# Performance work log

Hardware: AMD Instinct MI355X
Metric: run time of the kernel (lower is better)

The kernel has to match this reference:

```python
import jax, jax.numpy as jnp
import numpy as np

PLAYERS = 8
DMODEL = 256          # cfg.dmodel (per-embedding dim)
DK = 1024             # cfg.dk
WINDOW = 4096         # cfg.window == T here
A_SPACE = 64
DFULL = DMODEL * 2 * PLAYERS   # 4096, the concatenated model dim


def _positional_encoding(T, dmodel):
    # i = 1/10000^(2j/dmodel); pe[:, ::2]=sin(pos*i), pe[:, 1::2]=cos(pos*i)
    i = 1.0 / jnp.power(jnp.float32(10000.0), jnp.arange(0, dmodel, 2, dtype=jnp.float32) / dmodel)
    pos = jnp.arange(T, dtype=jnp.float32)[:, None]
    pe = jnp.zeros((T, dmodel), dtype=jnp.float32)
    pe = pe.at[:, ::2].set(jnp.sin(pos * i))
    pe = pe.at[:, 1::2].set(jnp.cos(pos * i))
    return pe


def setup_inputs() -> dict:
    key = jax.random.key(0)
    ks = jax.random.split(key, 12)
    n_rows = WINDOW * 2 * PLAYERS  # 65536 one-hot rows
    idx = jax.random.randint(ks[0], (n_rows,), 0, PLAYERS + 1)
    obs = jax.nn.one_hot(idx, PLAYERS + 1, dtype=jnp.int32)
    std = 2.0 / (5.0 * DFULL)  # torch.normal(0, var) uses var as std in the source
    return {
        "obs": obs,
        "o_emb": jax.random.normal(ks[1], (PLAYERS + 1, DMODEL), jnp.float32),
        "d_emb": jax.random.normal(ks[2], (PLAYERS + 1, DMODEL), jnp.float32),
        "WQ": jax.random.normal(ks[3], (DFULL, DK), jnp.float32) * std,
        "WK": jax.random.normal(ks[4], (DFULL, DK), jnp.float32) * std,
        "WV": jax.random.normal(ks[5], (DFULL, DK), jnp.float32) * std,
        "WO": jax.random.normal(ks[6], (DK, DK), jnp.float32) * std,
        "Wo_pol": jax.random.normal(ks[7], (A_SPACE, DK), jnp.float32) * 0.02,
        "bo_pol": jnp.zeros((A_SPACE,), jnp.float32),
        "Wd_pol": jax.random.normal(ks[8], (A_SPACE, DK), jnp.float32) * 0.02,
        "bd_pol": jnp.zeros((A_SPACE,), jnp.float32),
        "Wv": jax.random.normal(ks[9], (1, DK), jnp.float32) * 0.02,
        "bv": jnp.zeros((1,), jnp.float32),
    }


def reference(obs, o_emb, d_emb, WQ, WK, WV, WO, Wo_pol, bo_pol, Wd_pol, bd_pol, Wv, bv):
    obs2 = obs.reshape(-1, PLAYERS + 1)
    # torch.where(row == 1)[1] on one-hot rows == argmax
    idx_o = jnp.argmax(obs2[::2], axis=1)   # [T*players]
    idx_d = jnp.argmax(obs2[1::2], axis=1)  # [T*players]
    emb = jnp.concatenate([o_emb[idx_o], d_emb[idx_d]], axis=1)  # [T*players, 2*dmodel]
    x = emb.reshape(-1, DFULL) * jnp.sqrt(jnp.float32(DMODEL))    # [T, DFULL]
    T = x.shape[0]
    x = x + _positional_encoding(T, DFULL)
    q = x @ WQ  # [T, DK]
    k = x @ WK
    v = x @ WV
    att = jax.nn.softmax((q @ k.T) / jnp.sqrt(jnp.float32(DK)), axis=-1)  # [T, T]
    o = (att @ v) @ WO  # [T, DK]
    h = jax.nn.relu(o[-1])  # last position only, [DK]
    o_logits = h @ Wo_pol.T + bo_pol  # [A_SPACE]
    d_logits = h @ Wd_pol.T + bd_pol  # [A_SPACE]
    value = h @ Wv.T + bv             # [1]
    return (o_logits, d_logits, value)
```

## Files before the change

### kernel.cpp

```cpp
#include <hip/hip_runtime.h>
#include <stdint.h>

#define DK      1024
#define NBLK    256
#define NT      1024
#define NBAR    5u
#define LOG2_10000 13.287712379549449f

__device__ float g_e[4096];
__device__ float g_kq[4096];
__device__ float g_ol[1024];
__device__ float g_q8[2][8][1024];
__device__ float g_ctx8[2][8][1024];
__device__ float g_w8[2][8][160];

__device__ unsigned bar_gc[256];
__device__ unsigned bar_gm[32];
__device__ unsigned bar_gen;

__device__ __forceinline__ void stg(float* p, float v) {
    __hip_atomic_store(p, v, __ATOMIC_RELAXED, __HIP_MEMORY_SCOPE_AGENT);
}
__device__ __forceinline__ float lda(const float* p) {
    return __hip_atomic_load(p, __ATOMIC_RELAXED, __HIP_MEMORY_SCOPE_AGENT);
}

__device__ __forceinline__ void gbar_arrive(int bid, unsigned target) {
    asm volatile("s_waitcnt vmcnt(0)" ::: "memory");
    __syncthreads();
    if (threadIdx.x == 0) {
        unsigned g = (unsigned)bid & 7u;
        unsigned old = __hip_atomic_fetch_add(&bar_gc[g * 32], 1u,
                           __ATOMIC_RELAXED, __HIP_MEMORY_SCOPE_AGENT);
        if (old == target * 32u - 1u) {
            unsigned o2 = __hip_atomic_fetch_add(&bar_gm[0], 1u,
                              __ATOMIC_RELAXED, __HIP_MEMORY_SCOPE_AGENT);
            if (o2 == target * 8u - 1u)
                __hip_atomic_store(&bar_gen, target, __ATOMIC_RELEASE,
                                   __HIP_MEMORY_SCOPE_AGENT);
        }
    }
}
__device__ __forceinline__ void gbar_wait(unsigned target) {
    if (threadIdx.x == 0) {
        int gd = 0;
        while (__hip_atomic_load(&bar_gen, __ATOMIC_RELAXED,
                                 __HIP_MEMORY_SCOPE_AGENT) < target) {
            __builtin_amdgcn_s_sleep(1);
            if (++gd > (1 << 17)) break;
        }
    }
    __syncthreads();
}
__device__ __forceinline__ void gbar(int bid, unsigned target) {
    gbar_arrive(bid, target);
    gbar_wait(target);
}

__device__ __forceinline__ float4 bred4(float4 a, float* buf, int tid) {
    #pragma unroll
    for (int off = 32; off; off >>= 1) {
        a.x += __shfl_down(a.x, off, 64);
        a.y += __shfl_down(a.y, off, 64);
        a.z += __shfl_down(a.z, off, 64);
        a.w += __shfl_down(a.w, off, 64);
    }
    float4* b4 = (float4*)buf;
    if ((tid & 63) == 0) b4[tid >> 6] = a;
    __syncthreads();
    float4 r = {0.f, 0.f, 0.f, 0.f};
    if (tid == 0) {
        #pragma unroll
        for (int i = 0; i < 16; ++i) {
            float4 t = b4[i];
            r.x += t.x; r.y += t.y; r.z += t.z; r.w += t.w;
        }
    }
    __syncthreads();
    return r;
}

__global__ __launch_bounds__(1024, 4) void fused_k(
        const int*   __restrict__ obs,
        const float* __restrict__ o_emb,  const float* __restrict__ d_emb,
        const float* __restrict__ WQ,     const float* __restrict__ WK,
        const float* __restrict__ WV,     const float* __restrict__ WO,
        const float* __restrict__ Wo_pol, const float* __restrict__ bo_pol,
        const float* __restrict__ Wd_pol, const float* __restrict__ bd_pol,
        const float* __restrict__ Wv,     const float* __restrict__ bv,
        float* __restrict__ out,          char* __restrict__ ws) {
    (void)ws;

    __shared__ __align__(16) float smem[12416];
    float* axpeL = &smem[12288];
    unsigned char* sidx = (unsigned char*)&smem[12304];
    unsigned* sgen = (unsigned*)&smem[12400];

    int bid = blockIdx.x, tid = threadIdx.x;
    const int w  = ((bid & 7) << 5) | (bid >> 3);
    const int sh = bid & 7;
    const int lane = tid & 63;
    const int ksub = tid >> 8, n4 = tid & 255;

    if (tid == 0)
        *sgen = __hip_atomic_load(&bar_gen, __ATOMIC_RELAXED,
                                  __HIP_MEMORY_SCOPE_AGENT);

    const float4* WQ4 = (const float4*)WQ;
    float4 wqr[4];
    #pragma unroll
    for (int kk = 0; kk < 4; ++kk)
        wqr[kk] = WQ4[(size_t)(w * 16 + ksub * 4 + kk) * 256 + n4];

    int*   lidx = (int*)&smem[4100];
    float* lx   = &smem[4120];
    if (tid < 256) {
        int g = w * 256 + tid;
        const int* r = obs + (size_t)g * 9;
        int id = 0;
        #pragma unroll
        for (int j = 1; j < 9; ++j) id += j * r[j];
        sidx[(tid & ~15) | ((tid & 1) << 3) | ((tid >> 1) & 7)] =
            (unsigned char)id;
    }
    if (tid < 16) {
        const int* rr = obs + (size_t)(65520 + tid) * 9;
        int id2 = 0;
        #pragma unroll
        for (int j = 1; j < 9; ++j) id2 += j * rr[j];
        lidx[(tid & 1) * 8 + (tid >> 1)] = id2;
    }
    __syncthreads();
    const unsigned gen0 = *sgen;
    const int par = (int)((gen0 / NBAR) & 1u);
    float* q8  = &g_q8[par][0][0];
    float* c8  = &g_ctx8[par][0][0];
    float* w8  = &g_w8[par][0][0];
    {
        float* q8n = &g_q8[par ^ 1][0][0];
        float* c8n = &g_ctx8[par ^ 1][0][0];
        float* w8n = &g_w8[par ^ 1][0][0];
        if (tid < 69) {
            int idx = w * 69 + tid;
            if (idx < 8192)       stg(&q8n[idx], 0.0f);
            else if (idx < 16384) stg(&c8n[idx - 8192], 0.0f);
            else                  stg(&w8n[idx - 16384], 0.0f);
        }
    }
    if (tid < 16) {
        int c = w * 16 + tid;
        int p = c >> 9, rr = c & 511;
        const float* tab = (rr < 256) ? o_emb : d_emb;
        int slot = (rr < 256) ? p : 8 + p;
        int r2 = rr & 255;
        float e = tab[lidx[slot] * 256 + r2];
        float f = exp2f(-((float)(c & ~1) * (1.0f / 4096.0f)) * LOG2_10000);
        float sv, cv;
        __sincosf(4095.0f * f, &sv, &cv);
        lx[tid] = e * 16.0f + ((c & 1) ? cv : sv);
    }
    __syncthreads();
    {
        float4 acc = {0.f, 0.f, 0.f, 0.f};
        #pragma unroll
        for (int kk = 0; kk < 4; ++kk) {
            float xv = lx[ksub * 4 + kk];
            acc.x += xv * wqr[kk].x; acc.y += xv * wqr[kk].y;
            acc.z += xv * wqr[kk].z; acc.w += xv * wqr[kk].w;
        }
        float4* p4 = (float4*)smem;
        p4[ksub * 256 + n4] = acc;
        __syncthreads();
        if (tid < 256) {
            float4 a = p4[tid], b = p4[256 + tid],
                   c2 = p4[512 + tid], d = p4[768 + tid];
            float* dst = &q8[sh * 1024 + tid * 4];
            atomicAdd(dst + 0, a.x + b.x + c2.x + d.x);
            atomicAdd(dst + 1, a.y + b.y + c2.y + d.y);
            atomicAdd(dst + 2, a.z + b.z + c2.z + d.z);
            atomicAdd(dst + 3, a.w + b.w + c2.w + d.w);
        }
    }
    float4 wkr[4];
    {
        const float4* WKr = (const float4*)(WK + (size_t)(w * 16 + (tid >> 6)) * DK);
        #pragma unroll
        for (int i = 0; i < 4; ++i) wkr[i] = WKr[i * 64 + lane];
    }
    gbar_arrive(bid, gen0 + 1);
    {
        float* lemb = &smem[4096];
        float* lfrq = &smem[8724];
        for (int i = tid; i < 2048; i += NT)
            lfrq[i] = exp2f(-((float)(2 * i) * (1.0f / 4096.0f)) * LOG2_10000);
        for (int i = tid; i < 4608; i += NT) {
            int row = i >> 8, r = i & 255;
            lemb[row * 257 + r] = (row < 9) ? o_emb[row * 256 + r]
                                            : d_emb[(row - 9) * 256 + r];
        }
    }
    gbar_wait(gen0 + 1);

    {
        float* qsum = &smem[10772];
        float t = 0.0f;
        #pragma unroll
        for (int s2 = 0; s2 < 8; ++s2) t += lda(&q8[s2 * 1024 + tid]);
        qsum[tid] = t;
        __syncthreads();
        const float4* q4 = (const float4*)qsum;
        float acc = 0.0f;
        #pragma unroll
        for (int i = 0; i < 4; ++i) {
            float4 qq = q4[i * 64 + lane];
            acc += wkr[i].x * qq.x + wkr[i].y * qq.y
                 + wkr[i].z * qq.z + wkr[i].w * qq.w;
        }
        #pragma unroll
        for (int off = 32; off; off >>= 1) acc += __shfl_down(acc, off, 64);
        if (lane == 0) stg(&g_kq[w * 16 + (tid >> 6)], acc * (1.0f / 32.0f));
    }
    gbar(bid, gen0 + 2);

    {
        float* lkq   = smem;
        float* lemb  = &smem[4096];
        float* lfrq  = &smem[8724];
        float* ldot4 = &smem[10772];
        float* le16  = &smem[11360];
        float* lped  = &smem[11380];
        float* lh    = &smem[11400];
        #pragma unroll
        for (int i = 0; i < 4; ++i) {
            int c = tid + NT * i;
            lkq[c] = lda(&g_kq[c]);
        }
        if (tid < 144) lh[tid] = 0.0f;
        __syncthreads();
        if (tid < 576) {
            int p = tid >> 2, q = tid & 3;
            int sg = p / 9, id = p % 9;
            int base = (sg < 8) ? sg * 512 : (sg - 8) * 512 + 256;
            const float* e = lemb + ((sg < 8) ? id : (9 + id)) * 257;
            float a = 0.0f;
            for (int i = 0; i < 64; ++i) {
                int r = q * 64 + ((i + q * 13) & 63);
                a += e[r] * lkq[base + r];
            }
            ldot4[tid] = a;
        }
        {
            int tt = tid >> 6;
            int t = w * 16 + tt;
            float acc = 0.0f;
            #pragma unroll 4
            for (int jj = 0; jj < 32; ++jj) {
                int jf = jj * 64 + lane;
                float f = lfrq[jf];
                float svv, cvv;
                __sincosf((float)t * f, &svv, &cvv);
                acc += svv * lkq[2 * jf] + cvv * lkq[2 * jf + 1];
            }
            #pragma unroll
            for (int off = 32; off; off >>= 1) acc += __shfl_down(acc, off, 64);
            if (lane == 0) lped[tt] = acc;
        }
        __syncthreads();
        if (tid < 16) {
            float tot = lped[tid];
            const uint32_t* ip = (const uint32_t*)(sidx + tid * 16);
            uint32_t u0 = ip[0], u1 = ip[1], u2 = ip[2], u3 = ip[3];
            #pragma unroll
            for (int sg = 0; sg < 16; ++sg) {
                uint32_t u = (sg < 4) ? u0 : (sg < 8) ? u1 : (sg < 12) ? u2 : u3;
                int id = (u >> ((sg & 3) * 8)) & 0xFF;
                int p = (sg * 9 + id) * 4;
                tot += 16.0f * (ldot4[p] + ldot4[p + 1] + ldot4[p + 2] + ldot4[p + 3]);
            }
            float e = expf(tot);
            le16[tid] = e;
            stg(&g_e[w * 16 + tid], e);
        }
        __syncthreads();
        if (tid < 256) {
            int lt = tid >> 4, seg = tid & 15;
            int id = sidx[lt * 16 + seg];
            atomicAdd(&lh[seg * 9 + id], le16[lt]);
        }
        __syncthreads();
        if (tid < 144) atomicAdd(&w8[sh * 160 + tid], lh[tid]);
    }
    gbar(bid, gen0 + 3);

    float4 wvr[4];
    {
        const float4* WV4 = (const float4*)WV;
        #pragma unroll
        for (int kk = 0; kk < 4; ++kk)
            wvr[kk] = WV4[(size_t)(w * 16 + ksub * 4 + kk) * 256 + n4];
    }
    {
        float* le  = smem;
        float* pss = &smem[4352];
        float* psc = &smem[5376];
        float* lw  = &smem[6400];
        float* axv = &smem[6576];
        #pragma unroll
        for (int i = 0; i < 4; ++i) {
            int c = tid + NT * i;
            le[c] = lda(&g_e[c]);
        }
        if (tid < 144) {
            float s = 0.0f;
            #pragma unroll
            for (int s2 = 0; s2 < 8; ++s2) s += lda(&w8[s2 * 160 + tid]);
            lw[tid] = s;
        }
        __syncthreads();
        {
            int jl = tid >> 7, ts = tid & 127;
            int j = w * 8 + jl;
            float f = exp2f(-((float)(2 * j) * (1.0f / 4096.0f)) * LOG2_10000);
            float sf, cf;
            __sincosf(f, &sf, &cf);
            int t0 = ts * 32;
            float sv, cv;
            __sincosf((float)t0 * f, &sv, &cv);
            float ss = 0.f, sc = 0.f;
            #pragma unroll
            for (int i = 0; i < 32; ++i) {
                float a = le[t0 + i];
                ss += a * sv; sc += a * cv;
                float ns = sv * cf + cv * sf;
                cv = cv * cf - sv * sf;
                sv = ns;
            }
            pss[tid] = ss; psc[tid] = sc;
        }
        __syncthreads();
        if (tid < 512) {
            int m2 = tid >> 6, l = tid & 63;
            float a  = pss[m2 * 128 + l] + pss[m2 * 128 + 64 + l];
            float b2 = psc[m2 * 128 + l] + psc[m2 * 128 + 64 + l];
            #pragma unroll
            for (int off = 32; off; off >>= 1) {
                a  += __shfl_down(a, off, 64);
                b2 += __shfl_down(b2, off, 64);
            }
            if (l == 0) { axpeL[2 * m2] = a; axpeL[2 * m2 + 1] = b2; }
        }
        if (tid == 0) {
            float z = 0.0f;
            #pragma unroll
            for (int i = 0; i < 144; ++i) z += lw[i];
            smem[6560] = 16.0f / z;
        }
        __syncthreads();
        if (tid < 16) {
            int c = w * 16 + tid;
            int p = c >> 9, rr = c & 511;
            const float* tab = (rr < 256) ? o_emb : d_emb;
            int slot = (rr < 256) ? p : 8 + p;
            int r2 = rr & 255;
            float a = 0.0f;
            #pragma unroll
            for (int id2 = 0; id2 < 9; ++id2)
                a += lw[slot * 9 + id2] * tab[id2 * 256 + r2];
            axv[tid] = axpeL[tid] + 16.0f * a;
        }
        __syncthreads();
        {
            float4 acc = {0.f, 0.f, 0.f, 0.f};
            #pragma unroll
            for (int kk = 0; kk < 4; ++kk) {
                float av = axv[ksub * 4 + kk];
                acc.x += av * wvr[kk].x; acc.y += av * wvr[kk].y;
                acc.z += av * wvr[kk].z; acc.w += av * wvr[kk].w;
            }
            float4* p4 = (float4*)smem;
            p4[ksub * 256 + n4] = acc;
            __syncthreads();
            if (tid < 256) {
                float iz = smem[6560];
                float4 a = p4[tid], b = p4[256 + tid],
                       c2 = p4[512 + tid], d = p4[768 + tid];
                float* dst = &c8[sh * 1024 + tid * 4];
                atomicAdd(dst + 0, (a.x + b.x + c2.x + d.x) * iz);
                atomicAdd(dst + 1, (a.y + b.y + c2.y + d.y) * iz);
                atomicAdd(dst + 2, (a.z + b.z + c2.z + d.z) * iz);
                atomicAdd(dst + 3, (a.w + b.w + c2.w + d.w) * iz);
            }
        }
    }
    float4 wo = ((const float4*)WO)[(size_t)tid * 256 + w];
    gbar(bid, gen0 + 4);

    {
        float cj = 0.0f;
        #pragma unroll
        for (int s2 = 0; s2 < 8; ++s2) cj += lda(&c8[s2 * 1024 + tid]);
        float4 acc = {cj * wo.x, cj * wo.y, cj * wo.z, cj * wo.w};
        float4 s4 = bred4(acc, &smem[1024], tid);
        if (tid == 0) {
            stg(&g_ol[w * 4 + 0], s4.x); stg(&g_ol[w * 4 + 1], s4.y);
            stg(&g_ol[w * 4 + 2], s4.z); stg(&g_ol[w * 4 + 3], s4.w);
        }
    }
    float wvh = 0.0f, bh = 0.0f;
    if (w < 129) {
        const float* Wh;
        if (w < 64)       { Wh = Wo_pol + (size_t)w * DK;        bh = bo_pol[w]; }
        else if (w < 128) { Wh = Wd_pol + (size_t)(w - 64) * DK; bh = bd_pol[w - 64]; }
        else              { Wh = Wv;                              bh = bv[0]; }
        wvh = Wh[tid];
    }
    gbar(bid, gen0 + 5);

    if (w < 129) {
        float sacc = fmaxf(lda(&g_ol[tid]), 0.0f) * wvh;
        #pragma unroll
        for (int off = 32; off; off >>= 1) sacc += __shfl_down(sacc, off, 64);
        float* red = smem;
        if ((tid & 63) == 0) red[tid >> 6] = sacc;
        __syncthreads();
        if (tid == 0) {
            float tot = bh;
            #pragma unroll
            for (int i = 0; i < 16; ++i) tot += red[i];
            out[w] = tot;
        }
    }
}

extern "C" void kernel_launch(void* const* d_in, const int* in_sizes, int n_in,
                              void* d_out, int out_size, void* d_ws, size_t ws_size,
                              hipStream_t stream) {
    const int*   obs    = (const int*)  d_in[0];
    const float* o_emb  = (const float*)d_in[1];
    const float* d_emb  = (const float*)d_in[2];
    const float* WQ     = (const float*)d_in[3];
    const float* WK     = (const float*)d_in[4];
    const float* WV     = (const float*)d_in[5];
    const float* WO     = (const float*)d_in[6];
    const float* Wo_pol = (const float*)d_in[7];
    const float* bo_pol = (const float*)d_in[8];
    const float* Wd_pol = (const float*)d_in[9];
    const float* bd_pol = (const float*)d_in[10];
    const float* Wv     = (const float*)d_in[11];
    const float* bv     = (const float*)d_in[12];
    float* out = (float*)d_out;
    char* ws   = (char*)d_ws;

    fused_k<<<dim3(NBLK), dim3(NT), 0, stream>>>(
        obs, o_emb, d_emb, WQ, WK, WV, WO,
        Wo_pol, bo_pol, Wd_pol, bd_pol, Wv, bv, out, ws);
}
```

Before: 148.5 us.

## Split grid barriers to overlap weight loads and halve atomic partial shards

Splits each grid barrier into arrive and wait so the WK, WV, WO and head-weight loads run during the barrier wait instead of before it. Cuts the atomic reduction shards from 8 to 4, which halves the cross-block partial reads and the zeroing of the next parity buffer. Replaces the scalar cross-block loads with vectorized dwordx4 loads through inline asm that bypass the cache. Stores g_e transposed with padding in shared memory to avoid bank conflicts in the sin/cos projection loop. The trade-off is more atomic contention per shard, plus hand-written asm loads that wait on all outstanding memory operations.

```diff
diff --git a/kernel.cpp b/kernel.cpp
--- a/kernel.cpp
+++ b/kernel.cpp
@@ -7,12 +7,12 @@
 #define NBAR    5u
 #define LOG2_10000 13.287712379549449f
 
-__device__ float g_e[4096];
-__device__ float g_kq[4096];
-__device__ float g_ol[1024];
-__device__ float g_q8[2][8][1024];
-__device__ float g_ctx8[2][8][1024];
-__device__ float g_w8[2][8][160];
+__device__ __align__(16) float g_e[4096];
+__device__ __align__(16) float g_kq[4096];
+__device__ __align__(16) float g_ol[1024];
+__device__ __align__(16) float g_q8[2][4][1024];
+__device__ __align__(16) float g_ctx8[2][4][1024];
+__device__ __align__(16) float g_w8[2][4][160];
 
 __device__ unsigned bar_gc[256];
 __device__ unsigned bar_gm[32];
@@ -23,6 +23,24 @@
 }
 __device__ __forceinline__ float lda(const float* p) {
     return __hip_atomic_load(p, __ATOMIC_RELAXED, __HIP_MEMORY_SCOPE_AGENT);
+}
+__device__ __forceinline__ float4 ldv4(const float* p) {
+    float4 r;
+    asm volatile("global_load_dwordx4 %0, %1, off sc0 sc1\n\t"
+                 "s_waitcnt vmcnt(0)"
+                 : "=&v"(r) : "v"(p) : "memory");
+    return r;
+}
+__device__ __forceinline__ void ldv4x4(float4* r, const float* p0,
+                                       const float* p1, const float* p2,
+                                       const float* p3) {
+    asm volatile("global_load_dwordx4 %0, %4, off sc0 sc1\n\t"
+                 "global_load_dwordx4 %1, %5, off sc0 sc1\n\t"
+                 "global_load_dwordx4 %2, %6, off sc0 sc1\n\t"
+                 "global_load_dwordx4 %3, %7, off sc0 sc1\n\t"
+                 "s_waitcnt vmcnt(0)"
+                 : "=&v"(r[0]), "=&v"(r[1]), "=&v"(r[2]), "=&v"(r[3])
+                 : "v"(p0), "v"(p1), "v"(p2), "v"(p3) : "memory");
 }
 
 __device__ __forceinline__ void gbar_arrive(int bid, unsigned target) {
@@ -98,7 +116,7 @@
 
     int bid = blockIdx.x, tid = threadIdx.x;
     const int w  = ((bid & 7) << 5) | (bid >> 3);
-    const int sh = bid & 7;
+    const int sh = bid & 3;
     const int lane = tid & 63;
     const int ksub = tid >> 8, n4 = tid & 255;
 
@@ -133,18 +151,18 @@
     __syncthreads();
     const unsigned gen0 = *sgen;
     const int par = (int)((gen0 / NBAR) & 1u);
-    float* q8  = &g_q8[par][0][0];
-    float* c8  = &g_ctx8[par][0][0];
-    float* w8  = &g_w8[par][0][0];
+    float* q8 = &g_q8[par][0][0];
+    float* c8 = &g_ctx8[par][0][0];
+    float* w8 = &g_w8[par][0][0];
     {
         float* q8n = &g_q8[par ^ 1][0][0];
         float* c8n = &g_ctx8[par ^ 1][0][0];
         float* w8n = &g_w8[par ^ 1][0][0];
-        if (tid < 69) {
-            int idx = w * 69 + tid;
-            if (idx < 8192)       stg(&q8n[idx], 0.0f);
-            else if (idx < 16384) stg(&c8n[idx - 8192], 0.0f);
-            else                  stg(&w8n[idx - 16384], 0.0f);
+        if (tid < 35) {
+            int idx = w * 35 + tid;
+            if (idx < 4096)      stg(&q8n[idx], 0.0f);
+            else if (idx < 8192) stg(&c8n[idx - 4096], 0.0f);
+            else if (idx < 8832) stg(&w8n[idx - 8192], 0.0f);
         }
     }
     if (tid < 16) {
@@ -182,13 +200,11 @@
         }
     }
     float4 wkr[4];
+    gbar_arrive(bid, gen0 + 1);
     {
         const float4* WKr = (const float4*)(WK + (size_t)(w * 16 + (tid >> 6)) * DK);
         #pragma unroll
         for (int i = 0; i < 4; ++i) wkr[i] = WKr[i * 64 + lane];
-    }
-    gbar_arrive(bid, gen0 + 1);
-    {
         float* lemb = &smem[4096];
         float* lfrq = &smem[8724];
         for (int i = tid; i < 2048; i += NT)
@@ -203,10 +219,16 @@
 
     {
         float* qsum = &smem[10772];
-        float t = 0.0f;
-        #pragma unroll
-        for (int s2 = 0; s2 < 8; ++s2) t += lda(&q8[s2 * 1024 + tid]);
-        qsum[tid] = t;
+        if (tid < 256) {
+            float4 r[4];
+            ldv4x4(r, &q8[0 * 1024 + tid * 4], &q8[1 * 1024 + tid * 4],
+                      &q8[2 * 1024 + tid * 4], &q8[3 * 1024 + tid * 4]);
+            float4 s = { r[0].x + r[1].x + r[2].x + r[3].x,
+                         r[0].y + r[1].y + r[2].y + r[3].y,
+                         r[0].z + r[1].z + r[2].z + r[3].z,
+                         r[0].w + r[1].w + r[2].w + r[3].w };
+            ((float4*)qsum)[tid] = s;
+        }
         __syncthreads();
         const float4* q4 = (const float4*)qsum;
         float acc = 0.0f;
@@ -230,11 +252,7 @@
         float* le16  = &smem[11360];
         float* lped  = &smem[11380];
         float* lh    = &smem[11400];
-        #pragma unroll
-        for (int i = 0; i < 4; ++i) {
-            int c = tid + NT * i;
-            lkq[c] = lda(&g_kq[c]);
-        }
+        ((float4*)lkq)[tid] = ldv4(&g_kq[tid * 4]);
         if (tid < 144) lh[tid] = 0.0f;
         __syncthreads();
         if (tid < 576) {
@@ -290,31 +308,33 @@
         __syncthreads();
         if (tid < 144) atomicAdd(&w8[sh * 160 + tid], lh[tid]);
     }
-    gbar(bid, gen0 + 3);
-
     float4 wvr[4];
+    gbar_arrive(bid, gen0 + 3);
     {
         const float4* WV4 = (const float4*)WV;
         #pragma unroll
         for (int kk = 0; kk < 4; ++kk)
             wvr[kk] = WV4[(size_t)(w * 16 + ksub * 4 + kk) * 256 + n4];
     }
-    {
-        float* le  = smem;
+    gbar_wait(gen0 + 3);
+
+    {
+        float* leT = smem;
         float* pss = &smem[4352];
         float* psc = &smem[5376];
         float* lw  = &smem[6400];
         float* axv = &smem[6576];
-        #pragma unroll
-        for (int i = 0; i < 4; ++i) {
-            int c = tid + NT * i;
-            le[c] = lda(&g_e[c]);
+        {
+            float4 ev = ldv4(&g_e[tid * 4]);
+            int c0 = tid * 4, col = tid >> 3;
+            leT[((c0 + 0) & 31) * 129 + col] = ev.x;
+            leT[((c0 + 1) & 31) * 129 + col] = ev.y;
+            leT[((c0 + 2) & 31) * 129 + col] = ev.z;
+            leT[((c0 + 3) & 31) * 129 + col] = ev.w;
         }
         if (tid < 144) {
-            float s = 0.0f;
-            #pragma unroll
-            for (int s2 = 0; s2 < 8; ++s2) s += lda(&w8[s2 * 160 + tid]);
-            lw[tid] = s;
+            lw[tid] = lda(&w8[0 * 160 + tid]) + lda(&w8[1 * 160 + tid])
+                    + lda(&w8[2 * 160 + tid]) + lda(&w8[3 * 160 + tid]);
         }
         __syncthreads();
         {
@@ -329,7 +349,7 @@
             float ss = 0.f, sc = 0.f;
             #pragma unroll
             for (int i = 0; i < 32; ++i) {
-                float a = le[t0 + i];
+                float a = leT[i * 129 + ts];
                 ss += a * sv; sc += a * cv;
                 float ns = sv * cf + cv * sf;
                 cv = cv * cf - sv * sf;
@@ -392,13 +412,25 @@
             }
         }
     }
-    float4 wo = ((const float4*)WO)[(size_t)tid * 256 + w];
-    gbar(bid, gen0 + 4);
-
-    {
-        float cj = 0.0f;
-        #pragma unroll
-        for (int s2 = 0; s2 < 8; ++s2) cj += lda(&c8[s2 * 1024 + tid]);
+    float4 wo;
+    gbar_arrive(bid, gen0 + 4);
+    wo = ((const float4*)WO)[(size_t)tid * 256 + w];
+    gbar_wait(gen0 + 4);
+
+    {
+        float* lctx = smem;
+        if (tid < 256) {
+            float4 r[4];
+            ldv4x4(r, &c8[0 * 1024 + tid * 4], &c8[1 * 1024 + tid * 4],
+                      &c8[2 * 1024 + tid * 4], &c8[3 * 1024 + tid * 4]);
+            float4 s = { r[0].x + r[1].x + r[2].x + r[3].x,
+                         r[0].y + r[1].y + r[2].y + r[3].y,
+                         r[0].z + r[1].z + r[2].z + r[3].z,
+                         r[0].w + r[1].w + r[2].w + r[3].w };
+            ((float4*)lctx)[tid] = s;
+        }
+        __syncthreads();
+        float cj = lctx[tid];
         float4 acc = {cj * wo.x, cj * wo.y, cj * wo.z, cj * wo.w};
         float4 s4 = bred4(acc, &smem[1024], tid);
         if (tid == 0) {
@@ -407,6 +439,7 @@
         }
     }
     float wvh = 0.0f, bh = 0.0f;
+    gbar_arrive(bid, gen0 + 5);
     if (w < 129) {
         const float* Wh;
         if (w < 64)       { Wh = Wo_pol + (size_t)w * DK;        bh = bo_pol[w]; }
@@ -414,7 +447,7 @@
         else              { Wh = Wv;                              bh = bv[0]; }
         wvh = Wh[tid];
     }
-    gbar(bid, gen0 + 5);
+    gbar_wait(gen0 + 5);
 
     if (w < 129) {
         float sacc = fmaxf(lda(&g_ol[tid]), 0.0f) * wvh;
```

New measurement: 151.5 us. 1.02x slower.

## Split grid barriers to overlap weight prefetch and transpose e-buffer in LDS

Applied to the files above, without the earlier changes.

Several full grid barriers are split into arrive/wait pairs so the WK, WV, WO and head-weight loads are issued while other blocks are still reaching the barrier. The e-vector staging in shared memory is transposed with a padded stride of 129, so each thread's strided 32-element sweep reads without bank conflicts. A bounds guard is added on the zeroing of the double-buffered w8 scratch. The risk is that the prefetched registers stay live across the barrier wait, and that gbar_arrive's vmcnt(0) wait may already cover loads issued before it.

```diff
diff --git a/kernel.cpp b/kernel.cpp
--- a/kernel.cpp
+++ b/kernel.cpp
@@ -7,12 +7,12 @@
 #define NBAR    5u
 #define LOG2_10000 13.287712379549449f
 
-__device__ float g_e[4096];
-__device__ float g_kq[4096];
-__device__ float g_ol[1024];
-__device__ float g_q8[2][8][1024];
-__device__ float g_ctx8[2][8][1024];
-__device__ float g_w8[2][8][160];
+__device__ __align__(16) float g_e[4096];
+__device__ __align__(16) float g_kq[4096];
+__device__ __align__(16) float g_ol[1024];
+__device__ __align__(16) float g_q8[2][8][1024];
+__device__ __align__(16) float g_ctx8[2][8][1024];
+__device__ __align__(16) float g_w8[2][8][160];
 
 __device__ unsigned bar_gc[256];
 __device__ unsigned bar_gm[32];
@@ -133,9 +133,9 @@
     __syncthreads();
     const unsigned gen0 = *sgen;
     const int par = (int)((gen0 / NBAR) & 1u);
-    float* q8  = &g_q8[par][0][0];
-    float* c8  = &g_ctx8[par][0][0];
-    float* w8  = &g_w8[par][0][0];
+    float* q8 = &g_q8[par][0][0];
+    float* c8 = &g_ctx8[par][0][0];
+    float* w8 = &g_w8[par][0][0];
     {
         float* q8n = &g_q8[par ^ 1][0][0];
         float* c8n = &g_ctx8[par ^ 1][0][0];
@@ -144,7 +144,7 @@
             int idx = w * 69 + tid;
             if (idx < 8192)       stg(&q8n[idx], 0.0f);
             else if (idx < 16384) stg(&c8n[idx - 8192], 0.0f);
-            else                  stg(&w8n[idx - 16384], 0.0f);
+            else if (idx < 17664) stg(&w8n[idx - 16384], 0.0f);
         }
     }
     if (tid < 16) {
@@ -182,13 +182,11 @@
         }
     }
     float4 wkr[4];
+    gbar_arrive(bid, gen0 + 1);
     {
         const float4* WKr = (const float4*)(WK + (size_t)(w * 16 + (tid >> 6)) * DK);
         #pragma unroll
         for (int i = 0; i < 4; ++i) wkr[i] = WKr[i * 64 + lane];
-    }
-    gbar_arrive(bid, gen0 + 1);
-    {
         float* lemb = &smem[4096];
         float* lfrq = &smem[8724];
         for (int i = tid; i < 2048; i += NT)
@@ -290,25 +288,30 @@
         __syncthreads();
         if (tid < 144) atomicAdd(&w8[sh * 160 + tid], lh[tid]);
     }
-    gbar(bid, gen0 + 3);
-
     float4 wvr[4];
+    gbar_arrive(bid, gen0 + 3);
     {
         const float4* WV4 = (const float4*)WV;
         #pragma unroll
         for (int kk = 0; kk < 4; ++kk)
             wvr[kk] = WV4[(size_t)(w * 16 + ksub * 4 + kk) * 256 + n4];
     }
-    {
-        float* le  = smem;
+    gbar_wait(gen0 + 3);
+
+    {
+        float* leT = smem;
         float* pss = &smem[4352];
         float* psc = &smem[5376];
         float* lw  = &smem[6400];
         float* axv = &smem[6576];
-        #pragma unroll
-        for (int i = 0; i < 4; ++i) {
-            int c = tid + NT * i;
-            le[c] = lda(&g_e[c]);
+        {
+            int c0 = tid * 4, col = tid >> 3;
+            float e0 = lda(&g_e[c0 + 0]), e1 = lda(&g_e[c0 + 1]);
+            float e2 = lda(&g_e[c0 + 2]), e3 = lda(&g_e[c0 + 3]);
+            leT[((c0 + 0) & 31) * 129 + col] = e0;
+            leT[((c0 + 1) & 31) * 129 + col] = e1;
+            leT[((c0 + 2) & 31) * 129 + col] = e2;
+            leT[((c0 + 3) & 31) * 129 + col] = e3;
         }
         if (tid < 144) {
             float s = 0.0f;
@@ -329,7 +332,7 @@
             float ss = 0.f, sc = 0.f;
             #pragma unroll
             for (int i = 0; i < 32; ++i) {
-                float a = le[t0 + i];
+                float a = leT[i * 129 + ts];
                 ss += a * sv; sc += a * cv;
                 float ns = sv * cf + cv * sf;
                 cv = cv * cf - sv * sf;
@@ -392,8 +395,10 @@
             }
         }
     }
-    float4 wo = ((const float4*)WO)[(size_t)tid * 256 + w];
-    gbar(bid, gen0 + 4);
+    float4 wo;
+    gbar_arrive(bid, gen0 + 4);
+    wo = ((const float4*)WO)[(size_t)tid * 256 + w];
+    gbar_wait(gen0 + 4);
 
     {
         float cj = 0.0f;
@@ -407,6 +412,7 @@
         }
     }
     float wvh = 0.0f, bh = 0.0f;
+    gbar_arrive(bid, gen0 + 5);
     if (w < 129) {
         const float* Wh;
         if (w < 64)       { Wh = Wo_pol + (size_t)w * DK;        bh = bo_pol[w]; }
@@ -414,7 +420,7 @@
         else              { Wh = Wv;                              bh = bv[0]; }
         wvh = Wh[tid];
     }
-    gbar(bid, gen0 + 5);
+    gbar_wait(gen0 + 5);
 
     if (w < 129) {
         float sacc = fmaxf(lda(&g_ol[tid]), 0.0f) * wvh;
```

Result: no change. 148.8 us (+0.3%).
